# Optimization experiments

Measured on AMD Instinct MI355X. Metric: run time of the kernel, lower is better.

## Reference

```python
import jax, jax.numpy as jnp
import numpy as np


def setup_inputs() -> dict:
    key = jax.random.key(0)
    kq, kk, kv = jax.random.split(key, 3)
    B, H, S, D = 4, 16, 2048, 128
    return {
        "query": jax.random.normal(kq, (B, H, S, D), dtype=jnp.float32),
        "key": jax.random.normal(kk, (B, H, S, D), dtype=jnp.float32),
        "value": jax.random.normal(kv, (B, H, S, D), dtype=jnp.float32),
    }


def reference(query, key, value):
    # Faithful to RawSDP.forward with attn_mask=None, dropout_p=0, is_casual=False.
    head_dim = query.shape[-1]
    half_sqrt = jnp.asarray(np.sqrt(np.sqrt(head_dim)), dtype=query.dtype)
    q = query / half_sqrt
    k = key / half_sqrt
    # [B,H,Sq,Skv] attention logits (split scaling, as in original)
    attn_weight = jnp.einsum("bhqd,bhkd->bhqk", q, k)
    # softmax computed in float32, cast back to query dtype
    attn_weight = jax.nn.softmax(attn_weight.astype(jnp.float32), axis=-1).astype(query.dtype)
    return jnp.einsum("bhqk,bhkd->bhqd", attn_weight, value)
```

## Files before the change

kernel.cpp:

```cpp
#include <hip/hip_runtime.h>
#include <hip/hip_bf16.h>

typedef __attribute__((ext_vector_type(8))) short short8;
typedef __attribute__((ext_vector_type(4))) short short4_t;
typedef __attribute__((ext_vector_type(4))) float float4_t;

#define S_LEN 2048
#define D_DIM 128
#define BQ 128
#define BK 64
#define KS_STRIDE 136
#define VT_STRIDE 72
#define PS_STRIDE 72

__device__ __forceinline__ short f2bf(float f) {
    union { float f; unsigned u; } x; x.f = f;
    return (short)((x.u + 0x8000u) >> 16);
}

__device__ __forceinline__ float fast_exp2(float x) {
#if __has_builtin(__builtin_amdgcn_exp2f)
    return __builtin_amdgcn_exp2f(x);
#else
    return exp2f(x);
#endif
}

__global__ void __launch_bounds__(256, 2)
attn_fwd(const float* __restrict__ Q, const float* __restrict__ K,
         const float* __restrict__ V, float* __restrict__ Out)
{
    __shared__ __align__(16) short lds_k[BK * KS_STRIDE];
    __shared__ __align__(16) short lds_vt[D_DIM * VT_STRIDE];
    __shared__ __align__(16) short lds_p[4 * 32 * PS_STRIDE];

    const int qtile = blockIdx.x;
    const int bh    = blockIdx.y;
    const long base = (long)bh * S_LEN * D_DIM;
    const int t    = threadIdx.x;
    const int wave = t >> 6;
    const int lane = t & 63;
    const int ln   = lane & 15;
    const int quad = lane >> 4;

    const float qscale = 1.4426950408889634f / 11.313708498984761f;

    const int qrow0 = qtile * BQ + wave * 32;
    short8 qf[2][4];
    for (int rc = 0; rc < 2; ++rc)
        for (int ks = 0; ks < 4; ++ks) {
            const float* p = Q + base + (long)(qrow0 + 16 * rc + ln) * D_DIM + 32 * ks + 8 * quad;
            float4_t a = *(const float4_t*)p;
            float4_t b = *(const float4_t*)(p + 4);
            short8 f;
            f[0] = f2bf(a[0] * qscale); f[1] = f2bf(a[1] * qscale);
            f[2] = f2bf(a[2] * qscale); f[3] = f2bf(a[3] * qscale);
            f[4] = f2bf(b[0] * qscale); f[5] = f2bf(b[1] * qscale);
            f[6] = f2bf(b[2] * qscale); f[7] = f2bf(b[3] * qscale);
            qf[rc][ks] = f;
        }

    float4_t o[2][8];
    for (int rc = 0; rc < 2; ++rc)
        for (int nc = 0; nc < 8; ++nc) { o[rc][nc][0]=0.f; o[rc][nc][1]=0.f; o[rc][nc][2]=0.f; o[rc][nc][3]=0.f; }
    float lsum[2][4];
    for (int rc = 0; rc < 2; ++rc)
        for (int r = 0; r < 4; ++r) lsum[rc][r] = 0.f;

    const int pbase = wave * 32 * PS_STRIDE;

    const int kd0 = (t & 31) << 2;
    const int ksr = t >> 5;
    const int vs  = t & 63;
    const int vdb = (t >> 6) * 32;
    float4_t kbuf[8], vbuf[8];
    for (int r = 0; r < 8; ++r)
        kbuf[r] = *(const float4_t*)(K + base + (long)(ksr + 8 * r) * D_DIM + kd0);
    for (int r = 0; r < 8; ++r)
        vbuf[r] = *(const float4_t*)(V + base + (long)vs * D_DIM + vdb + 4 * r);

    for (int kv0 = 0; kv0 < S_LEN; kv0 += BK) {
        __syncthreads();

        for (int r = 0; r < 8; ++r) {
            short4_t w4;
            w4[0] = f2bf(kbuf[r][0]); w4[1] = f2bf(kbuf[r][1]);
            w4[2] = f2bf(kbuf[r][2]); w4[3] = f2bf(kbuf[r][3]);
            *(short4_t*)&lds_k[(ksr + 8 * r) * KS_STRIDE + kd0] = w4;
        }
        for (int r = 0; r < 8; ++r) {
            const int d0 = vdb + 4 * r;
            lds_vt[(d0 + 0) * VT_STRIDE + vs] = f2bf(vbuf[r][0]);
            lds_vt[(d0 + 1) * VT_STRIDE + vs] = f2bf(vbuf[r][1]);
            lds_vt[(d0 + 2) * VT_STRIDE + vs] = f2bf(vbuf[r][2]);
            lds_vt[(d0 + 3) * VT_STRIDE + vs] = f2bf(vbuf[r][3]);
        }

        {
            const int nk = (kv0 + BK) & (S_LEN - 1);
            for (int r = 0; r < 8; ++r)
                kbuf[r] = *(const float4_t*)(K + base + (long)(nk + ksr + 8 * r) * D_DIM + kd0);
            for (int r = 0; r < 8; ++r)
                vbuf[r] = *(const float4_t*)(V + base + (long)(nk + vs) * D_DIM + vdb + 4 * r);
        }

        __syncthreads();

        float4_t sacc[2][4];
        for (int rc = 0; rc < 2; ++rc)
            for (int nc = 0; nc < 4; ++nc) { sacc[rc][nc][0]=0.f; sacc[rc][nc][1]=0.f; sacc[rc][nc][2]=0.f; sacc[rc][nc][3]=0.f; }
        for (int ks = 0; ks < 4; ++ks)
            for (int nc = 0; nc < 4; ++nc) {
                short8 bk_ = *(const short8*)&lds_k[(16 * nc + ln) * KS_STRIDE + 32 * ks + 8 * quad];
                sacc[0][nc] = __builtin_amdgcn_mfma_f32_16x16x32_bf16(qf[0][ks], bk_, sacc[0][nc], 0, 0, 0);
                sacc[1][nc] = __builtin_amdgcn_mfma_f32_16x16x32_bf16(qf[1][ks], bk_, sacc[1][nc], 0, 0, 0);
            }

        for (int rc = 0; rc < 2; ++rc) {
            const int rbase = 16 * rc + 4 * quad;
            for (int nc = 0; nc < 4; ++nc) {
                const int cb = pbase + 16 * nc + ln;
                float p0 = fast_exp2(sacc[rc][nc][0]);
                float p1 = fast_exp2(sacc[rc][nc][1]);
                float p2 = fast_exp2(sacc[rc][nc][2]);
                float p3 = fast_exp2(sacc[rc][nc][3]);
                lsum[rc][0] += p0; lsum[rc][1] += p1;
                lsum[rc][2] += p2; lsum[rc][3] += p3;
                lds_p[cb + (rbase + 0) * PS_STRIDE] = f2bf(p0);
                lds_p[cb + (rbase + 1) * PS_STRIDE] = f2bf(p1);
                lds_p[cb + (rbase + 2) * PS_STRIDE] = f2bf(p2);
                lds_p[cb + (rbase + 3) * PS_STRIDE] = f2bf(p3);
            }
        }

        __asm__ volatile("s_waitcnt lgkmcnt(0)" ::: "memory");

        for (int ks = 0; ks < 2; ++ks) {
            short8 ap0 = *(const short8*)&lds_p[pbase + (ln)      * PS_STRIDE + 32 * ks + 8 * quad];
            short8 ap1 = *(const short8*)&lds_p[pbase + (16 + ln) * PS_STRIDE + 32 * ks + 8 * quad];
            for (int nc = 0; nc < 8; ++nc) {
                short8 bv = *(const short8*)&lds_vt[(16 * nc + ln) * VT_STRIDE + 32 * ks + 8 * quad];
                o[0][nc] = __builtin_amdgcn_mfma_f32_16x16x32_bf16(ap0, bv, o[0][nc], 0, 0, 0);
                o[1][nc] = __builtin_amdgcn_mfma_f32_16x16x32_bf16(ap1, bv, o[1][nc], 0, 0, 0);
            }
        }
    }

    for (int rc = 0; rc < 2; ++rc)
        for (int r = 0; r < 4; ++r) {
            float s = lsum[rc][r];
            s += __shfl_xor(s, 1);
            s += __shfl_xor(s, 2);
            s += __shfl_xor(s, 4);
            s += __shfl_xor(s, 8);
            const float inv = 1.0f / s;
            const int row = qrow0 + 16 * rc + 4 * quad + r;
            float* po = Out + base + (long)row * D_DIM;
            for (int nc = 0; nc < 8; ++nc)
                po[16 * nc + ln] = o[rc][nc][r] * inv;
        }
}

extern "C" void kernel_launch(void* const* d_in, const int* in_sizes, int n_in,
                              void* d_out, int out_size, void* d_ws, size_t ws_size,
                              hipStream_t stream) {
    (void)in_sizes; (void)n_in; (void)d_ws; (void)ws_size; (void)out_size;
    const float* Q = (const float*)d_in[0];
    const float* K = (const float*)d_in[1];
    const float* V = (const float*)d_in[2];
    float* Out = (float*)d_out;
    dim3 grid(S_LEN / BQ, 64, 1);
    dim3 block(256, 1, 1);
    attn_fwd<<<grid, block, 0, stream>>>(Q, K, V, Out);
}
```

Baseline: 383.0 us.

## Compute transposed S so P stays in registers, feed PV via f16 MFMA

The QK^T MFMA operands are swapped so each lane holds S^T fragments whose layout matches the A-operand of the 16x16x16 f16 MFMA. P can then go straight from registers into the PV product, removing the LDS round-trip for P and its wait. V is now staged in LDS as f16 with paired half2 writes instead of scalar bf16 transposed writes. In exchange, PV uses the smaller-K f16 MFMA, which needs twice as many instructions, and the row-sum reduction changes to cross-quad shuffles.

```diff
diff --git a/kernel.cpp b/kernel.cpp
--- a/kernel.cpp
+++ b/kernel.cpp
@@ -4,6 +4,8 @@
 typedef __attribute__((ext_vector_type(8))) short short8;
 typedef __attribute__((ext_vector_type(4))) short short4_t;
 typedef __attribute__((ext_vector_type(4))) float float4_t;
+typedef __attribute__((ext_vector_type(4))) _Float16 half4_t;
+typedef __attribute__((ext_vector_type(2))) _Float16 half2_t;
 
 #define S_LEN 2048
 #define D_DIM 128
@@ -11,7 +13,6 @@
 #define BK 64
 #define KS_STRIDE 136
 #define VT_STRIDE 72
-#define PS_STRIDE 72
 
 __device__ __forceinline__ short f2bf(float f) {
     union { float f; unsigned u; } x; x.f = f;
@@ -30,9 +31,8 @@
 attn_fwd(const float* __restrict__ Q, const float* __restrict__ K,
          const float* __restrict__ V, float* __restrict__ Out)
 {
-    __shared__ __align__(16) short lds_k[BK * KS_STRIDE];
-    __shared__ __align__(16) short lds_vt[D_DIM * VT_STRIDE];
-    __shared__ __align__(16) short lds_p[4 * 32 * PS_STRIDE];
+    __shared__ __align__(16) short    lds_k[BK * KS_STRIDE];
+    __shared__ __align__(16) _Float16 lds_vt[D_DIM * VT_STRIDE];
 
     const int qtile = blockIdx.x;
     const int bh    = blockIdx.y;
@@ -47,9 +47,9 @@
 
     const int qrow0 = qtile * BQ + wave * 32;
     short8 qf[2][4];
-    for (int rc = 0; rc < 2; ++rc)
+    for (int nt = 0; nt < 2; ++nt)
         for (int ks = 0; ks < 4; ++ks) {
-            const float* p = Q + base + (long)(qrow0 + 16 * rc + ln) * D_DIM + 32 * ks + 8 * quad;
+            const float* p = Q + base + (long)(qrow0 + 16 * nt + ln) * D_DIM + 32 * ks + 8 * quad;
             float4_t a = *(const float4_t*)p;
             float4_t b = *(const float4_t*)(p + 4);
             short8 f;
@@ -57,27 +57,25 @@
             f[2] = f2bf(a[2] * qscale); f[3] = f2bf(a[3] * qscale);
             f[4] = f2bf(b[0] * qscale); f[5] = f2bf(b[1] * qscale);
             f[6] = f2bf(b[2] * qscale); f[7] = f2bf(b[3] * qscale);
-            qf[rc][ks] = f;
+            qf[nt][ks] = f;
         }
 
     float4_t o[2][8];
-    for (int rc = 0; rc < 2; ++rc)
-        for (int nc = 0; nc < 8; ++nc) { o[rc][nc][0]=0.f; o[rc][nc][1]=0.f; o[rc][nc][2]=0.f; o[rc][nc][3]=0.f; }
-    float lsum[2][4];
-    for (int rc = 0; rc < 2; ++rc)
-        for (int r = 0; r < 4; ++r) lsum[rc][r] = 0.f;
-
-    const int pbase = wave * 32 * PS_STRIDE;
+    for (int qt = 0; qt < 2; ++qt)
+        for (int nc = 0; nc < 8; ++nc) { o[qt][nc][0]=0.f; o[qt][nc][1]=0.f; o[qt][nc][2]=0.f; o[qt][nc][3]=0.f; }
+    float lsum[2] = {0.f, 0.f};
 
     const int kd0 = (t & 31) << 2;
     const int ksr = t >> 5;
-    const int vs  = t & 63;
-    const int vdb = (t >> 6) * 32;
-    float4_t kbuf[8], vbuf[8];
+    const int vj  = t & 31;
+    const int vd0 = (t >> 5) << 4;
+    float4_t kbuf[8], va[4], vb[4];
     for (int r = 0; r < 8; ++r)
         kbuf[r] = *(const float4_t*)(K + base + (long)(ksr + 8 * r) * D_DIM + kd0);
-    for (int r = 0; r < 8; ++r)
-        vbuf[r] = *(const float4_t*)(V + base + (long)vs * D_DIM + vdb + 4 * r);
+    for (int r = 0; r < 4; ++r) {
+        va[r] = *(const float4_t*)(V + base + (long)(2 * vj)     * D_DIM + vd0 + 4 * r);
+        vb[r] = *(const float4_t*)(V + base + (long)(2 * vj + 1) * D_DIM + vd0 + 4 * r);
+    }
 
     for (int kv0 = 0; kv0 < S_LEN; kv0 += BK) {
         __syncthreads();
@@ -88,76 +86,70 @@
             w4[2] = f2bf(kbuf[r][2]); w4[3] = f2bf(kbuf[r][3]);
             *(short4_t*)&lds_k[(ksr + 8 * r) * KS_STRIDE + kd0] = w4;
         }
-        for (int r = 0; r < 8; ++r) {
-            const int d0 = vdb + 4 * r;
-            lds_vt[(d0 + 0) * VT_STRIDE + vs] = f2bf(vbuf[r][0]);
-            lds_vt[(d0 + 1) * VT_STRIDE + vs] = f2bf(vbuf[r][1]);
-            lds_vt[(d0 + 2) * VT_STRIDE + vs] = f2bf(vbuf[r][2]);
-            lds_vt[(d0 + 3) * VT_STRIDE + vs] = f2bf(vbuf[r][3]);
-        }
+        for (int r = 0; r < 4; ++r)
+            for (int c = 0; c < 4; ++c) {
+                half2_t h2; h2[0] = (_Float16)va[r][c]; h2[1] = (_Float16)vb[r][c];
+                *(half2_t*)&lds_vt[(vd0 + 4 * r + c) * VT_STRIDE + 2 * vj] = h2;
+            }
 
         {
             const int nk = (kv0 + BK) & (S_LEN - 1);
             for (int r = 0; r < 8; ++r)
                 kbuf[r] = *(const float4_t*)(K + base + (long)(nk + ksr + 8 * r) * D_DIM + kd0);
-            for (int r = 0; r < 8; ++r)
-                vbuf[r] = *(const float4_t*)(V + base + (long)(nk + vs) * D_DIM + vdb + 4 * r);
+            for (int r = 0; r < 4; ++r) {
+                va[r] = *(const float4_t*)(V + base + (long)(nk + 2 * vj)     * D_DIM + vd0 + 4 * r);
+                vb[r] = *(const float4_t*)(V + base + (long)(nk + 2 * vj + 1) * D_DIM + vd0 + 4 * r);
+            }
         }
 
         __syncthreads();
 
-        float4_t sacc[2][4];
-        for (int rc = 0; rc < 2; ++rc)
-            for (int nc = 0; nc < 4; ++nc) { sacc[rc][nc][0]=0.f; sacc[rc][nc][1]=0.f; sacc[rc][nc][2]=0.f; sacc[rc][nc][3]=0.f; }
+        float4_t sacc[4][2];
+        for (int mt = 0; mt < 4; ++mt)
+            for (int nt = 0; nt < 2; ++nt) { sacc[mt][nt][0]=0.f; sacc[mt][nt][1]=0.f; sacc[mt][nt][2]=0.f; sacc[mt][nt][3]=0.f; }
         for (int ks = 0; ks < 4; ++ks)
-            for (int nc = 0; nc < 4; ++nc) {
-                short8 bk_ = *(const short8*)&lds_k[(16 * nc + ln) * KS_STRIDE + 32 * ks + 8 * quad];
-                sacc[0][nc] = __builtin_amdgcn_mfma_f32_16x16x32_bf16(qf[0][ks], bk_, sacc[0][nc], 0, 0, 0);
-                sacc[1][nc] = __builtin_amdgcn_mfma_f32_16x16x32_bf16(qf[1][ks], bk_, sacc[1][nc], 0, 0, 0);
+            for (int mt = 0; mt < 4; ++mt) {
+                short8 ak = *(const short8*)&lds_k[(16 * mt + ln) * KS_STRIDE + 32 * ks + 8 * quad];
+                sacc[mt][0] = __builtin_amdgcn_mfma_f32_16x16x32_bf16(ak, qf[0][ks], sacc[mt][0], 0, 0, 0);
+                sacc[mt][1] = __builtin_amdgcn_mfma_f32_16x16x32_bf16(ak, qf[1][ks], sacc[mt][1], 0, 0, 0);
             }
 
-        for (int rc = 0; rc < 2; ++rc) {
-            const int rbase = 16 * rc + 4 * quad;
-            for (int nc = 0; nc < 4; ++nc) {
-                const int cb = pbase + 16 * nc + ln;
-                float p0 = fast_exp2(sacc[rc][nc][0]);
-                float p1 = fast_exp2(sacc[rc][nc][1]);
-                float p2 = fast_exp2(sacc[rc][nc][2]);
-                float p3 = fast_exp2(sacc[rc][nc][3]);
-                lsum[rc][0] += p0; lsum[rc][1] += p1;
-                lsum[rc][2] += p2; lsum[rc][3] += p3;
-                lds_p[cb + (rbase + 0) * PS_STRIDE] = f2bf(p0);
-                lds_p[cb + (rbase + 1) * PS_STRIDE] = f2bf(p1);
-                lds_p[cb + (rbase + 2) * PS_STRIDE] = f2bf(p2);
-                lds_p[cb + (rbase + 3) * PS_STRIDE] = f2bf(p3);
+        half4_t af[4][2];
+        for (int mt = 0; mt < 4; ++mt)
+            for (int nt = 0; nt < 2; ++nt) {
+                float p0 = fast_exp2(sacc[mt][nt][0]);
+                float p1 = fast_exp2(sacc[mt][nt][1]);
+                float p2 = fast_exp2(sacc[mt][nt][2]);
+                float p3 = fast_exp2(sacc[mt][nt][3]);
+                lsum[nt] += (p0 + p1) + (p2 + p3);
+                half4_t h; h[0] = (_Float16)p0; h[1] = (_Float16)p1;
+                h[2] = (_Float16)p2; h[3] = (_Float16)p3;
+                af[mt][nt] = h;
             }
-        }
 
-        __asm__ volatile("s_waitcnt lgkmcnt(0)" ::: "memory");
-
-        for (int ks = 0; ks < 2; ++ks) {
-            short8 ap0 = *(const short8*)&lds_p[pbase + (ln)      * PS_STRIDE + 32 * ks + 8 * quad];
-            short8 ap1 = *(const short8*)&lds_p[pbase + (16 + ln) * PS_STRIDE + 32 * ks + 8 * quad];
+        for (int mt = 0; mt < 4; ++mt)
             for (int nc = 0; nc < 8; ++nc) {
-                short8 bv = *(const short8*)&lds_vt[(16 * nc + ln) * VT_STRIDE + 32 * ks + 8 * quad];
-                o[0][nc] = __builtin_amdgcn_mfma_f32_16x16x32_bf16(ap0, bv, o[0][nc], 0, 0, 0);
-                o[1][nc] = __builtin_amdgcn_mfma_f32_16x16x32_bf16(ap1, bv, o[1][nc], 0, 0, 0);
+                half4_t bv = *(const half4_t*)&lds_vt[(16 * nc + ln) * VT_STRIDE + 16 * mt + 4 * quad];
+                o[0][nc] = __builtin_amdgcn_mfma_f32_16x16x16f16(af[mt][0], bv, o[0][nc], 0, 0, 0);
+                o[1][nc] = __builtin_amdgcn_mfma_f32_16x16x16f16(af[mt][1], bv, o[1][nc], 0, 0, 0);
             }
-        }
     }
 
-    for (int rc = 0; rc < 2; ++rc)
+    float fullsum[2];
+    for (int nt = 0; nt < 2; ++nt) {
+        float s = lsum[nt];
+        s += __shfl_xor(s, 16);
+        s += __shfl_xor(s, 32);
+        fullsum[nt] = s;
+    }
+    for (int qt = 0; qt < 2; ++qt)
         for (int r = 0; r < 4; ++r) {
-            float s = lsum[rc][r];
-            s += __shfl_xor(s, 1);
-            s += __shfl_xor(s, 2);
-            s += __shfl_xor(s, 4);
-            s += __shfl_xor(s, 8);
-            const float inv = 1.0f / s;
-            const int row = qrow0 + 16 * rc + 4 * quad + r;
+            const float den = __shfl(fullsum[qt], 4 * quad + r);
+            const float inv = 1.0f / den;
+            const int row = qrow0 + 16 * qt + 4 * quad + r;
             float* po = Out + base + (long)row * D_DIM;
             for (int nc = 0; nc < 8; ++nc)
-                po[16 * nc + ln] = o[rc][nc][r] * inv;
+                po[16 * nc + ln] = o[qt][nc][r] * inv;
         }
 }
 
```

After: 402.3 us. +5.0%, slower.
